# Optimization experiments

Measured on AMD Instinct MI355X. Metric: run time of the kernel, lower is better.

## Reference

```python
import jax, jax.numpy as jnp
import numpy as np

N = 50000        # nodes
E = 600000       # edges (no self-loops; reference adds N self-loops)
IN_C = 64
OUT_C = 64
HEADS = 2
NEG_SLOPE = 0.2  # GraphLayer default negative_slope
BN_EPS = 1e-5


def setup_inputs() -> dict:
    key = jax.random.key(0)
    ks = jax.random.split(key, 14)
    x = jax.random.normal(ks[0], (N, IN_C), dtype=jnp.float32)
    # edge_index with no self-loops by construction (original calls remove_self_loops)
    src = jax.random.randint(ks[1], (E,), 0, N, dtype=jnp.int32)
    off = jax.random.randint(ks[2], (E,), 1, N, dtype=jnp.int32)
    dst = (src + off) % N
    edge_index = jnp.stack([src, dst])  # [2, E]
    embedding = jax.random.normal(ks[3], (N, OUT_C), dtype=jnp.float32)
    s = 0.1
    lin_w = jax.random.normal(ks[4], (IN_C, HEADS * OUT_C), dtype=jnp.float32) * s
    att_i = jax.random.normal(ks[5], (1, HEADS, OUT_C), dtype=jnp.float32) * s
    att_j = jax.random.normal(ks[6], (1, HEADS, OUT_C), dtype=jnp.float32) * s
    att_em_i = jax.random.normal(ks[7], (1, HEADS, OUT_C), dtype=jnp.float32) * s
    att_em_j = jax.random.normal(ks[8], (1, HEADS, OUT_C), dtype=jnp.float32) * s
    gnn_bias = jnp.zeros((HEADS * OUT_C,), dtype=jnp.float32)
    ff_w = jax.random.normal(ks[9], (HEADS * OUT_C, OUT_C), dtype=jnp.float32) * s
    ff_b = jnp.zeros((OUT_C,), dtype=jnp.float32)
    bn_gamma = jnp.ones((OUT_C,), dtype=jnp.float32)
    bn_beta = jnp.zeros((OUT_C,), dtype=jnp.float32)
    return {"x": x, "edge_index": edge_index, "embedding": embedding,
            "lin_w": lin_w, "att_i": att_i, "att_j": att_j,
            "att_em_i": att_em_i, "att_em_j": att_em_j, "gnn_bias": gnn_bias,
            "ff_w": ff_w, "ff_b": ff_b, "bn_gamma": bn_gamma, "bn_beta": bn_beta}


def reference(x, edge_index, embedding, lin_w, att_i, att_j, att_em_i, att_em_j,
              gnn_bias, ff_w, ff_b, bn_gamma, bn_beta):
    n = x.shape[0]
    h = (x @ lin_w).reshape(n, HEADS, OUT_C)  # lin projection, per-head view
    # add self-loops (input already has none)
    ar = jnp.arange(n, dtype=edge_index.dtype)
    ei = jnp.concatenate([edge_index, jnp.stack([ar, ar])], axis=1)
    src, dst = ei[0], ei[1]                   # x_j = source, x_i = target
    x_i, x_j = h[dst], h[src]                 # [Et, H, C]
    emb_i = embedding[dst][:, None, :]        # [Et, 1, C] broadcast over heads
    emb_j = embedding[src][:, None, :]
    # alpha = <cat(x_i,emb_i), cat(att_i,att_em_i)> + <cat(x_j,emb_j), cat(att_j,att_em_j)>
    alpha = ((x_i * att_i[0]).sum(-1) + (emb_i * att_em_i[0]).sum(-1)
             + (x_j * att_j[0]).sum(-1) + (emb_j * att_em_j[0]).sum(-1))  # [Et, H]
    alpha = jax.nn.leaky_relu(alpha, NEG_SLOPE)
    # segment softmax over incoming edges of each target node (PyG softmax)
    amax = jax.ops.segment_max(alpha, dst, num_segments=n)
    ex = jnp.exp(alpha - amax[dst])
    denom = jax.ops.segment_sum(ex, dst, num_segments=n)
    alpha = ex / (denom[dst] + 1e-16)
    out = jax.ops.segment_sum(x_j * alpha[:, :, None], dst, num_segments=n)  # [n,H,C]
    out = out.reshape(n, HEADS * OUT_C) + gnn_bias  # concat heads + bias
    out = out @ ff_w + ff_b                         # self.ff
    mean = out.mean(axis=0)                          # BatchNorm1d, training stats
    var = out.var(axis=0)                            # biased variance (torch BN)
    out = (out - mean) / jnp.sqrt(var + BN_EPS) * bn_gamma + bn_beta
    return jax.nn.relu(out)
```

## Files before the change

### kernel.cpp

```cpp
#include <hip/hip_runtime.h>

#define C 64
#define HC 128
#define NEG 0.2f

typedef __attribute__((ext_vector_type(8))) short bf16x8;
typedef __attribute__((ext_vector_type(4))) float f32x4;
typedef __fp16 fp16x2 __attribute__((ext_vector_type(2)));

__device__ __forceinline__ float lrelu(float v) { return v >= 0.f ? v : NEG * v; }
__device__ __forceinline__ unsigned short f2bf(float f) {
    unsigned u = __float_as_uint(f);
    return (unsigned short)((u + 0x7fffu + ((u >> 16) & 1u)) >> 16);
}
__device__ __forceinline__ float bflo(unsigned u) { return __uint_as_float(u << 16); }
__device__ __forceinline__ float bfhi(unsigned u) { return __uint_as_float(u & 0xffff0000u); }

__global__ __launch_bounds__(256) void k_prep(
    const float* __restrict__ lin_w, const float* __restrict__ ff_w,
    bf16x8* __restrict__ linb, bf16x8* __restrict__ ffb,
    int* __restrict__ deg_counter, int nz)
{
    const int i = blockIdx.x * 256 + threadIdx.x;
    if (i < nz) deg_counter[i] = 0;
    if (i < 1024) {
        const int lane = i & 63, frag = i >> 6;
        const int r = lane & 15, g = lane >> 4;
        const int m4 = frag >> 2, p = (frag >> 1) & 1, kk = frag & 1;
        bf16x8 bb;
#pragma unroll
        for (int j = 0; j < 8; ++j)
            bb[j] = (short)f2bf(lin_w[(kk * 32 + 8 * g + j) * HC + 32 * m4 + 2 * r + p]);
        linb[i] = bb;
    } else if (i < 2048) {
        const int i2 = i - 1024;
        const int lane = i2 & 63, frag = i2 >> 6;
        const int r = lane & 15, g = lane >> 4;
        const int w = frag >> 2, kk = frag & 3;
        bf16x8 bb;
#pragma unroll
        for (int j = 0; j < 8; ++j)
            bb[j] = (short)f2bf(ff_w[(kk * 32 + 8 * g + j) * C + w * 16 + r]);
        ffb[i2] = bb;
    }
}

__global__ __launch_bounds__(256) void kA_mfma_edge(
    const float* __restrict__ x, const bf16x8* __restrict__ linb,
    const float* __restrict__ emb,
    const float* __restrict__ att_i, const float* __restrict__ att_j,
    const float* __restrict__ att_em_i, const float* __restrict__ att_em_j,
    unsigned* __restrict__ hb, float2* __restrict__ a_i2,
    float2* __restrict__ a_j2, int n_nodes, int nb64,
    const int* __restrict__ dstv, int* __restrict__ deg,
    int* __restrict__ rank, int e)
{
    const int t = threadIdx.x;
    if (blockIdx.x >= nb64) {
        const int i = (blockIdx.x - nb64) * 256 + t;
        if (i < e) rank[i] = atomicAdd(&deg[dstv[i]], 1);
        return;
    }
    __shared__ __align__(16) char smem[8192];
    const int lane = t & 63, w = t >> 6;
    const int r = lane & 15, g = lane >> 4;

    bf16x8 B[4][2][2];
#pragma unroll
    for (int m4 = 0; m4 < 4; ++m4)
#pragma unroll
        for (int p = 0; p < 2; ++p)
#pragma unroll
            for (int kk = 0; kk < 2; ++kk)
                B[m4][p][kk] = linb[(m4 * 4 + p * 2 + kk) * 64 + lane];

    float wi[4][2], wj[4][2];
#pragma unroll
    for (int m4 = 0; m4 < 4; ++m4)
#pragma unroll
        for (int p = 0; p < 2; ++p) {
            wi[m4][p] = att_i[32 * m4 + 2 * r + p];
            wj[m4][p] = att_j[32 * m4 + 2 * r + p];
        }
    float wem_i0[4], wem_i1[4], wem_j0[4], wem_j1[4];
#pragma unroll
    for (int q = 0; q < 4; ++q) {
        wem_i0[q] = att_em_i[q * 16 + r];
        wem_i1[q] = att_em_i[64 + q * 16 + r];
        wem_j0[q] = att_em_j[q * 16 + r];
        wem_j1[q] = att_em_j[64 + q * 16 + r];
    }

    {
        const int row = t >> 2, q = t & 3;
        const int gn = blockIdx.x * 64 + row;
        float ff[16];
        if (gn < n_nodes) {
            const float4* xs = (const float4*)(x + (size_t)gn * C + q * 16);
            *(float4*)&ff[0] = xs[0]; *(float4*)&ff[4] = xs[1];
            *(float4*)&ff[8] = xs[2]; *(float4*)&ff[12] = xs[3];
        } else {
#pragma unroll
            for (int j = 0; j < 16; ++j) ff[j] = 0.f;
        }
        bf16x8 p0, p1;
#pragma unroll
        for (int j = 0; j < 8; ++j) {
            p0[j] = (short)f2bf(ff[j]);
            p1[j] = (short)f2bf(ff[8 + j]);
        }
        const unsigned bb = (unsigned)((row >> 4) * 2048 + (row & 15) * 128 + q * 32);
        const unsigned sw = (unsigned)((row & 7) << 4);
        *(bf16x8*)(smem + ((bb) ^ sw)) = p0;
        *(bf16x8*)(smem + ((bb + 16) ^ sw)) = p1;
    }
    __syncthreads();

    bf16x8 A[2];
    const unsigned ab = (unsigned)(w * 2048 + r * 128 + g * 16);
    const unsigned sw = (unsigned)((r & 7) << 4);
    A[0] = *(const bf16x8*)(smem + ((ab) ^ sw));
    A[1] = *(const bf16x8*)(smem + ((ab + 64) ^ sw));

    f32x4 acc[4][2];
#pragma unroll
    for (int m4 = 0; m4 < 4; ++m4)
#pragma unroll
        for (int p = 0; p < 2; ++p) acc[m4][p] = (f32x4){0.f, 0.f, 0.f, 0.f};
#pragma unroll
    for (int kk = 0; kk < 2; ++kk)
#pragma unroll
        for (int m4 = 0; m4 < 4; ++m4)
#pragma unroll
            for (int p = 0; p < 2; ++p)
                acc[m4][p] = __builtin_amdgcn_mfma_f32_16x16x32_bf16(A[kk], B[m4][p][kk], acc[m4][p], 0, 0, 0);

    const int nb = blockIdx.x * 64 + w * 16 + 4 * g;
#pragma unroll
    for (int j = 0; j < 4; ++j) {
        const int rr = nb + j;
        if (rr < n_nodes) {
            float pi0 = 0.f, pi1 = 0.f, pj0 = 0.f, pj1 = 0.f;
            unsigned* hp = hb + (size_t)rr * 64 + r;
#pragma unroll
            for (int m4 = 0; m4 < 4; ++m4) {
                const float ev = acc[m4][0][j], ov = acc[m4][1][j];
                hp[m4 * 16] = ((unsigned)f2bf(ov) << 16) | (unsigned)f2bf(ev);
                if (m4 < 2) {
                    pi0 = fmaf(ev, wi[m4][0], fmaf(ov, wi[m4][1], pi0));
                    pj0 = fmaf(ev, wj[m4][0], fmaf(ov, wj[m4][1], pj0));
                } else {
                    pi1 = fmaf(ev, wi[m4][0], fmaf(ov, wi[m4][1], pi1));
                    pj1 = fmaf(ev, wj[m4][0], fmaf(ov, wj[m4][1], pj1));
                }
            }
#pragma unroll
            for (int q = 0; q < 4; ++q) {
                const float ev = emb[(size_t)rr * C + q * 16 + r];
                pi0 = fmaf(ev, wem_i0[q], pi0);
                pi1 = fmaf(ev, wem_i1[q], pi1);
                pj0 = fmaf(ev, wem_j0[q], pj0);
                pj1 = fmaf(ev, wem_j1[q], pj1);
            }
#pragma unroll
            for (int m = 1; m < 16; m <<= 1) {
                pi0 += __shfl_xor(pi0, m, 64);
                pi1 += __shfl_xor(pi1, m, 64);
                pj0 += __shfl_xor(pj0, m, 64);
                pj1 += __shfl_xor(pj1, m, 64);
            }
            if (r == 0) {
                a_i2[rr] = make_float2(pi0, pi1);
                a_j2[rr] = make_float2(pj0, pj1);
            }
        }
    }
}

__global__ __launch_bounds__(256) void k_scan(
    const int* __restrict__ deg, int* __restrict__ counter,
    int* __restrict__ rowptr, int n)
{
    __shared__ int sh[256];
    __shared__ int s_base;
    const int t = threadIdx.x;
    const int i0 = blockIdx.x * 512 + t * 2;
    const int a = (i0 < n) ? deg[i0] : 0;
    const int b = (i0 + 1 < n) ? deg[i0 + 1] : 0;
    const int s = a + b;
    sh[t] = s;
    __syncthreads();
    for (int off = 1; off < 256; off <<= 1) {
        int v = (t >= off) ? sh[t - off] : 0;
        __syncthreads();
        sh[t] += v;
        __syncthreads();
    }
    const int excl = sh[t] - s;
    if (t == 255) s_base = atomicAdd(counter, sh[255]);
    __syncthreads();
    const int base = s_base;
    if (i0 < n)     rowptr[i0]     = base + excl;
    if (i0 + 1 < n) rowptr[i0 + 1] = base + excl + a;
}

__global__ __launch_bounds__(256) void k_fill(
    const int* __restrict__ srcv, const int* __restrict__ dstv,
    const int* __restrict__ rank, const int* __restrict__ rowptr,
    const float2* __restrict__ a_i2, const float2* __restrict__ a_j2,
    int2* __restrict__ edata, int e)
{
    int i = blockIdx.x * 256 + threadIdx.x;
    if (i >= e) return;
    const int s = srcv[i], d = dstv[i];
    const float2 ai = a_i2[d];
    const float2 aj = a_j2[s];
    const float ex0 = __expf(lrelu(ai.x + aj.x));
    const float ex1 = __expf(lrelu(ai.y + aj.y));
    union { fp16x2 h; int u; } cv;
    cv.h = __builtin_amdgcn_cvt_pkrtz(ex0, ex1);
    edata[rowptr[d] + rank[i]] = make_int2(s, cv.u);
}

__global__ __launch_bounds__(256) void kD_gff(
    const int2* __restrict__ edata, const int* __restrict__ rowptr,
    const int* __restrict__ deg, const unsigned* __restrict__ hb,
    const float2* __restrict__ a_i2, const float2* __restrict__ a_j2,
    const float2* __restrict__ bias2, const bf16x8* __restrict__ ffb,
    const float* __restrict__ ff_b, float* __restrict__ out2,
    float* __restrict__ partial, int n_nodes)
{
    __shared__ __align__(16) char smem[4096];
    const int t = threadIdx.x;
    const int lane = t & 63, w = t >> 6;
    const int r = lane & 15, g = lane >> 4;

    bf16x8 B[4];
#pragma unroll
    for (int kk = 0; kk < 4; ++kk) B[kk] = ffb[(w * 4 + kk) * 64 + lane];
    const float fb = ff_b[w * 16 + r];
    const float2 bv = bias2[lane];

    const int nbase = blockIdx.x * 16;
#pragma unroll
    for (int j = 0; j < 4; ++j) {
        const int n = nbase + w * 4 + j;
        unsigned packed = 0;
        if (n < n_nodes) {
            const int r0 = __builtin_amdgcn_readfirstlane(rowptr[n]);
            const int r1 = r0 + __builtin_amdgcn_readfirstlane(deg[n]);
            const float2 ai = a_i2[n];
            const float2 ajs = a_j2[n];
            const float es0 = __expf(lrelu(ai.x + ajs.x));
            const float es1 = __expf(lrelu(ai.y + ajs.y));
            float den0 = es0, den1 = es1;
            const unsigned hv = hb[(size_t)n * 64 + lane];
            const float exs = (lane < 32) ? es0 : es1;
            float2 acc = make_float2(exs * bflo(hv), exs * bfhi(hv));
#pragma unroll 4
            for (int rr = r0; rr < r1; ++rr) {
                const int2 ed = edata[rr];
                const int se = ed.x;
                union { int u; fp16x2 h; } cv; cv.u = ed.y;
                const float ex0 = (float)cv.h[0];
                const float ex1 = (float)cv.h[1];
                den0 += ex0; den1 += ex1;
                const float exh = (lane < 32) ? ex0 : ex1;
                const unsigned v = hb[(size_t)se * 64 + lane];
                acc.x = fmaf(exh, bflo(v), acc.x);
                acc.y = fmaf(exh, bfhi(v), acc.y);
            }
            const float den = (lane < 32) ? den0 : den1;
            const float inv = 1.f / (den + 1e-16f);
            packed = ((unsigned)f2bf(fmaf(acc.y, inv, bv.y)) << 16)
                   | (unsigned)f2bf(fmaf(acc.x, inv, bv.x));
        }
        const int row = w * 4 + j;
        const unsigned byte = (unsigned)(row * 256 + lane * 4);
        *(unsigned*)(smem + (byte ^ ((unsigned)(row & 7) << 4))) = packed;
    }
    __syncthreads();

    bf16x8 A[4];
#pragma unroll
    for (int kk = 0; kk < 4; ++kk) {
        const unsigned byte = (unsigned)(r * 256 + kk * 64 + g * 16);
        A[kk] = *(const bf16x8*)(smem + (byte ^ ((unsigned)(r & 7) << 4)));
    }
    f32x4 acc4 = (f32x4){0.f, 0.f, 0.f, 0.f};
#pragma unroll
    for (int kk = 0; kk < 4; ++kk)
        acc4 = __builtin_amdgcn_mfma_f32_16x16x32_bf16(A[kk], B[kk], acc4, 0, 0, 0);

    float st = 0.f, st2 = 0.f;
#pragma unroll
    for (int jj = 0; jj < 4; ++jj) {
        const int rr = nbase + 4 * g + jj;
        if (rr < n_nodes) {
            const float v = acc4[jj] + fb;
            out2[(size_t)rr * C + w * 16 + r] = v;
            st += v; st2 = fmaf(v, v, st2);
        }
    }
    st  += __shfl_xor(st, 16, 64);  st  += __shfl_xor(st, 32, 64);
    st2 += __shfl_xor(st2, 16, 64); st2 += __shfl_xor(st2, 32, 64);
    if (g == 0) {
        partial[(size_t)blockIdx.x * 128 + w * 16 + r] = st;
        partial[(size_t)blockIdx.x * 128 + 64 + w * 16 + r] = st2;
    }
}

__global__ __launch_bounds__(256) void k5_red(
    const float* __restrict__ partial, float* __restrict__ colsum,
    float* __restrict__ colsq, int nblk)
{
    __shared__ float sh[256];
    const int c = blockIdx.x;
    const int t = threadIdx.x;
    float s = 0.f;
    for (int b = t; b < nblk; b += 256) s += partial[(size_t)b * 128 + c];
    sh[t] = s;
    __syncthreads();
    for (int off = 128; off; off >>= 1) {
        if (t < off) sh[t] += sh[t + off];
        __syncthreads();
    }
    if (t == 0) {
        if (c < C) colsum[c] = sh[0];
        else       colsq[c - C] = sh[0];
    }
}

__global__ __launch_bounds__(256) void k6_bn(
    float* __restrict__ out2, const float* __restrict__ colsum,
    const float* __restrict__ colsq, const float* __restrict__ gamma,
    const float* __restrict__ beta, float inv_n, int total )
{
    int i = blockIdx.x * 256 + threadIdx.x;
    if (i >= total) return;
    int c = i & 63;
    float mean = colsum[c] * inv_n;
    float var = colsq[c] * inv_n - mean * mean;
    float rstd = rsqrtf(var + 1e-5f);
    float v = (out2[i] - mean) * rstd * gamma[c] + beta[c];
    out2[i] = fmaxf(v, 0.f);
}

extern "C" void kernel_launch(void* const* d_in, const int* in_sizes, int n_in,
                              void* d_out, int out_size, void* d_ws, size_t ws_size,
                              hipStream_t stream)
{
    const float* x        = (const float*)d_in[0];
    const int*   ei       = (const int*)d_in[1];
    const float* emb      = (const float*)d_in[2];
    const float* lin_w    = (const float*)d_in[3];
    const float* att_i    = (const float*)d_in[4];
    const float* att_j    = (const float*)d_in[5];
    const float* att_em_i = (const float*)d_in[6];
    const float* att_em_j = (const float*)d_in[7];
    const float* gnn_bias = (const float*)d_in[8];
    const float* ff_w     = (const float*)d_in[9];
    const float* ff_b     = (const float*)d_in[10];
    const float* bn_g     = (const float*)d_in[11];
    const float* bn_b     = (const float*)d_in[12];

    const int n = in_sizes[0] / C;
    const int e = in_sizes[1] / 2;
    const int* srcv = ei;
    const int* dstv = ei + e;

    const int nb64 = (n + 63) / 64;
    const int nb16 = (n + 15) / 16;
    const int nbE  = (e + 255) / 256;

    float* ws = (float*)d_ws;
    unsigned* hb      = (unsigned*)ws;
    bf16x8*   linb    = (bf16x8*)(hb + (size_t)n * 64);
    bf16x8*   ffb     = linb + 1024;
    float*    a_if    = (float*)(ffb + 1024);
    float*    a_jf    = a_if + 2 * (size_t)n;
    float*    partial = a_jf + 2 * (size_t)n;
    float*    colsum  = partial + (size_t)nb16 * 128;
    float*    colsq   = colsum + C;
    int*      deg     = (int*)(colsq + C);
    int*      counter = deg + n;
    int*      rowptr  = counter + 2;
    int*      rank    = rowptr + n;
    int2*     edata   = (int2*)(rank + e);
    float*    out2    = (float*)d_out;

    k_prep<<<(n + 2 + 255) / 256, 256, 0, stream>>>(lin_w, ff_w, linb, ffb,
                                                    deg, n + 2);
    kA_mfma_edge<<<nb64 + nbE, 256, 0, stream>>>(
        x, linb, emb, att_i, att_j, att_em_i, att_em_j,
        hb, (float2*)a_if, (float2*)a_jf, n, nb64, dstv, deg, rank, e);
    k_scan<<<(n + 511) / 512, 256, 0, stream>>>(deg, counter, rowptr, n);
    k_fill<<<nbE, 256, 0, stream>>>(srcv, dstv, rank, rowptr,
                                    (const float2*)a_if, (const float2*)a_jf,
                                    edata, e);
    kD_gff<<<nb16, 256, 0, stream>>>(edata, rowptr, deg, hb,
                                     (const float2*)a_if, (const float2*)a_jf,
                                     (const float2*)gnn_bias, ffb, ff_b,
                                     out2, partial, n);
    k5_red<<<128, 256, 0, stream>>>(partial, colsum, colsq, nb16);
    {
        int total = n * C;
        k6_bn<<<(total + 255) / 256, 256, 0, stream>>>(out2, colsum, colsq, bn_g, bn_b,
                                                       1.0f / (float)n, total);
    }
}
```

Baseline: 190.7 us.

## Split degree counters into 8 slices by edge index for sorted CSR fill

Edge degree counting now uses 8 separate counter arrays chosen by bits of the edge index, so each slice is filled by a contiguous range of edges. The scan combines the slices into total degree and per-slice offsets, and the fill writes edges slice by slice. Within each node's row, edges from earlier index ranges come first, which improves locality of the edata writes and of the later neighbour gathers. The cost is zeroing and scanning 8x more counter memory and writing per-slice offsets.

```diff
diff --git a/kernel.cpp b/kernel.cpp
--- a/kernel.cpp
+++ b/kernel.cpp
@@ -52,13 +52,16 @@
     const float* __restrict__ att_em_i, const float* __restrict__ att_em_j,
     unsigned* __restrict__ hb, float2* __restrict__ a_i2,
     float2* __restrict__ a_j2, int n_nodes, int nb64,
-    const int* __restrict__ dstv, int* __restrict__ deg,
+    const int* __restrict__ dstv, int* __restrict__ degS,
     int* __restrict__ rank, int e)
 {
     const int t = threadIdx.x;
     if (blockIdx.x >= nb64) {
         const int i = (blockIdx.x - nb64) * 256 + t;
-        if (i < e) rank[i] = atomicAdd(&deg[dstv[i]], 1);
+        if (i < e) {
+            const int s = (i >> 16) & 7;
+            rank[i] = atomicAdd(&degS[s * n_nodes + dstv[i]], 1);
+        }
         return;
     }
     __shared__ __align__(16) char smem[8192];
@@ -178,17 +181,24 @@
 }
 
 __global__ __launch_bounds__(256) void k_scan(
-    const int* __restrict__ deg, int* __restrict__ counter,
-    int* __restrict__ rowptr, int n)
+    const int* __restrict__ degS, int* __restrict__ counter,
+    int* __restrict__ rowptr, int* __restrict__ degt,
+    int* __restrict__ xoff, int n)
 {
     __shared__ int sh[256];
     __shared__ int s_base;
     const int t = threadIdx.x;
     const int i0 = blockIdx.x * 512 + t * 2;
-    const int a = (i0 < n) ? deg[i0] : 0;
-    const int b = (i0 + 1 < n) ? deg[i0 + 1] : 0;
-    const int s = a + b;
-    sh[t] = s;
+    int d0[8], d1[8];
+    int t0 = 0, t1 = 0;
+#pragma unroll
+    for (int s = 0; s < 8; ++s) {
+        d0[s] = (i0 < n) ? degS[s * n + i0] : 0;
+        d1[s] = (i0 + 1 < n) ? degS[s * n + i0 + 1] : 0;
+        t0 += d0[s]; t1 += d1[s];
+    }
+    const int tot = t0 + t1;
+    sh[t] = tot;
     __syncthreads();
     for (int off = 1; off < 256; off <<= 1) {
         int v = (t >= off) ? sh[t - off] : 0;
@@ -196,35 +206,46 @@
         sh[t] += v;
         __syncthreads();
     }
-    const int excl = sh[t] - s;
+    const int excl = sh[t] - tot;
     if (t == 255) s_base = atomicAdd(counter, sh[255]);
     __syncthreads();
     const int base = s_base;
-    if (i0 < n)     rowptr[i0]     = base + excl;
-    if (i0 + 1 < n) rowptr[i0 + 1] = base + excl + a;
+    if (i0 < n) {
+        int run = base + excl;
+        rowptr[i0] = run; degt[i0] = t0;
+#pragma unroll
+        for (int s = 0; s < 8; ++s) { xoff[s * n + i0] = run; run += d0[s]; }
+    }
+    if (i0 + 1 < n) {
+        int run = base + excl + t0;
+        rowptr[i0 + 1] = run; degt[i0 + 1] = t1;
+#pragma unroll
+        for (int s = 0; s < 8; ++s) { xoff[s * n + i0 + 1] = run; run += d1[s]; }
+    }
 }
 
 __global__ __launch_bounds__(256) void k_fill(
     const int* __restrict__ srcv, const int* __restrict__ dstv,
-    const int* __restrict__ rank, const int* __restrict__ rowptr,
+    const int* __restrict__ rank, const int* __restrict__ xoff,
     const float2* __restrict__ a_i2, const float2* __restrict__ a_j2,
-    int2* __restrict__ edata, int e)
+    int2* __restrict__ edata, int e, int n)
 {
     int i = blockIdx.x * 256 + threadIdx.x;
     if (i >= e) return;
     const int s = srcv[i], d = dstv[i];
+    const int sl = (i >> 16) & 7;
     const float2 ai = a_i2[d];
     const float2 aj = a_j2[s];
     const float ex0 = __expf(lrelu(ai.x + aj.x));
     const float ex1 = __expf(lrelu(ai.y + aj.y));
     union { fp16x2 h; int u; } cv;
     cv.h = __builtin_amdgcn_cvt_pkrtz(ex0, ex1);
-    edata[rowptr[d] + rank[i]] = make_int2(s, cv.u);
+    edata[xoff[sl * n + d] + rank[i]] = make_int2(s, cv.u);
 }
 
 __global__ __launch_bounds__(256) void kD_gff(
     const int2* __restrict__ edata, const int* __restrict__ rowptr,
-    const int* __restrict__ deg, const unsigned* __restrict__ hb,
+    const int* __restrict__ degt, const unsigned* __restrict__ hb,
     const float2* __restrict__ a_i2, const float2* __restrict__ a_j2,
     const float2* __restrict__ bias2, const bf16x8* __restrict__ ffb,
     const float* __restrict__ ff_b, float* __restrict__ out2,
@@ -248,7 +269,7 @@
         unsigned packed = 0;
         if (n < n_nodes) {
             const int r0 = __builtin_amdgcn_readfirstlane(rowptr[n]);
-            const int r1 = r0 + __builtin_amdgcn_readfirstlane(deg[n]);
+            const int r1 = r0 + __builtin_amdgcn_readfirstlane(degt[n]);
             const float2 ai = a_i2[n];
             const float2 ajs = a_j2[n];
             const float es0 = __expf(lrelu(ai.x + ajs.x));
@@ -382,23 +403,27 @@
     float*    partial = a_jf + 2 * (size_t)n;
     float*    colsum  = partial + (size_t)nb16 * 128;
     float*    colsq   = colsum + C;
-    int*      deg     = (int*)(colsq + C);
-    int*      counter = deg + n;
+    int*      degS    = (int*)(colsq + C);
+    int*      counter = degS + 8 * (size_t)n;
     int*      rowptr  = counter + 2;
-    int*      rank    = rowptr + n;
+    int*      degt    = rowptr + n;
+    int*      xoff    = degt + n;
+    int*      rank    = xoff + 8 * (size_t)n;
     int2*     edata   = (int2*)(rank + e);
     float*    out2    = (float*)d_out;
 
-    k_prep<<<(n + 2 + 255) / 256, 256, 0, stream>>>(lin_w, ff_w, linb, ffb,
-                                                    deg, n + 2);
+    const int nz = 8 * n + 2;
+    k_prep<<<(nz + 255) / 256, 256, 0, stream>>>(lin_w, ff_w, linb, ffb,
+                                                 degS, nz);
     kA_mfma_edge<<<nb64 + nbE, 256, 0, stream>>>(
         x, linb, emb, att_i, att_j, att_em_i, att_em_j,
-        hb, (float2*)a_if, (float2*)a_jf, n, nb64, dstv, deg, rank, e);
-    k_scan<<<(n + 511) / 512, 256, 0, stream>>>(deg, counter, rowptr, n);
-    k_fill<<<nbE, 256, 0, stream>>>(srcv, dstv, rank, rowptr,
+        hb, (float2*)a_if, (float2*)a_jf, n, nb64, dstv, degS, rank, e);
+    k_scan<<<(n + 511) / 512, 256, 0, stream>>>(degS, counter, rowptr, degt,
+                                                xoff, n);
+    k_fill<<<nbE, 256, 0, stream>>>(srcv, dstv, rank, xoff,
                                     (const float2*)a_if, (const float2*)a_jf,
-                                    edata, e);
-    kD_gff<<<nb16, 256, 0, stream>>>(edata, rowptr, deg, hb,
+                                    edata, e, n);
+    kD_gff<<<nb16, 256, 0, stream>>>(edata, rowptr, degt, hb,
                                      (const float2*)a_if, (const float2*)a_jf,
                                      (const float2*)gnn_bias, ffb, ff_b,
                                      out2, partial, n);
```

After: 189.3 us. No clear change (-0.7%).
